# Performance work log

Hardware: AMD Instinct MI355X
Metric: run time of the kernel (lower is better)

The kernel has to match this reference:

```python
import jax, jax.numpy as jnp
import numpy as np


def setup_inputs() -> dict:
    key = jax.random.key(0)
    k1, k2 = jax.random.split(key)
    B, H, W, E = 8, 32, 32, 256   # latent grid (NHWC layout, as in vector_quantize)
    N_E = 16384                   # codebook size
    x = jax.random.normal(k1, (B, H, W, E), dtype=jnp.float32)
    codebook = jax.random.normal(k2, (N_E, E), dtype=jnp.float32)
    return {"x": x, "codebook": codebook}


def reference(x, codebook):
    # d[b,h,w,k] = ||x[b,h,w] - codebook[k]||^2 (expanded form, as in source)
    x_sq = jnp.sum(x * x, axis=-1, keepdims=True)            # [B,H,W,1]
    cb_sq = jnp.sum(codebook * codebook, axis=1)              # [N_E]
    cross = jnp.einsum('bhwe,ke->bhwk', x, codebook)          # [B,H,W,N_E]
    d = x_sq + cb_sq - 2.0 * cross
    indices = jnp.argmin(d, axis=-1)                          # [B,H,W]
    x_q = jnp.take(codebook, indices, axis=0)                 # one-hot @ codebook == row gather
    # straight-through / ReplaceGrad: forward value is x_q, gradient flows to x
    return x + jax.lax.stop_gradient(x_q - x)
```

## Files before the change

kernel.cpp:

```cpp
#include <hip/hip_runtime.h>
#include <stdint.h>

#define M_PIX 8192
#define N_CB  16384
#define KD    256

typedef float f32x4 __attribute__((ext_vector_type(4)));
typedef int   i32x4 __attribute__((ext_vector_type(4)));
typedef int   i32x8 __attribute__((ext_vector_type(8)));
typedef unsigned long long ull;

#define OFF_CF8  (0ULL)
#define OFF_XF8  (4ULL << 20)
#define OFF_CBSQ (6ULL << 20)
#define OFF_SLOT (7ULL << 20)
#define WS_REQ   (15ULL << 20)

__device__ __forceinline__ unsigned int fkey(float s) {
  unsigned int f = __float_as_uint(s);
  return f ^ ((unsigned int)(((int)f) >> 31) | 0x80000000u);
}
__device__ __forceinline__ unsigned char f2e4m3(float v) {
  float av = fminf(fabsf(v), 448.0f);
  const unsigned s = (__float_as_uint(v) >> 24) & 0x80u;
  unsigned m;
  if (av >= 0.015625f) {
    unsigned u = __float_as_uint(av);
    u += 0x7FFFFu + ((u >> 20) & 1u);
    m = (((u >> 23) - 120u) << 3) | ((u >> 20) & 7u);
  } else {
    m = (unsigned)(int)rintf(av * 512.0f);
  }
  return (unsigned char)(s | m);
}
__device__ __forceinline__ void gl_lds16(const unsigned char* g, char* l) {
  __builtin_amdgcn_global_load_lds(
      (const __attribute__((address_space(1))) unsigned int*)(const void*)g,
      (__attribute__((address_space(3))) unsigned int*)(void*)l,
      16, 0, 0);
}
__device__ __forceinline__ void ins2f(float k, float& v1, float& v2) {
  v2 = fminf(v2, fmaxf(v1, k));
  v1 = fminf(v1, k);
}
__device__ __forceinline__ i32x8 ld32(const char* p, int addr) {
  const i32x4 lo = *(const i32x4*)(const void*)(p + addr);
  const i32x4 hi = *(const i32x4*)(const void*)(p + (addr ^ 16));
  return (i32x8){lo.x, lo.y, lo.z, lo.w, hi.x, hi.y, hi.z, hi.w};
}

__global__ __launch_bounds__(256) void prep_kernel(
    const float* __restrict__ x, const float* __restrict__ cb,
    unsigned char* __restrict__ Cf8, unsigned char* __restrict__ Xf8,
    float* __restrict__ cbsq) {
  const int wid = threadIdx.x >> 6, lane = threadIdx.x & 63;
  const int row = blockIdx.x * 4 + wid;
  const bool isCb = (row < N_CB);
  const int rowL = isCb ? row : row - N_CB;
  const float* src = (isCb ? cb : x) + (size_t)rowL * KD;
  const float4 v = ((const float4*)src)[lane];
  uchar4 pk;
  pk.x = f2e4m3(v.x); pk.y = f2e4m3(v.y); pk.z = f2e4m3(v.z); pk.w = f2e4m3(v.w);
  *(uchar4*)(void*)((isCb ? Cf8 : Xf8) + (size_t)rowL * KD + lane * 4) = pk;
  if (isCb) {
    float ss = v.x*v.x + v.y*v.y + v.z*v.z + v.w*v.w;
    #pragma unroll
    for (int off = 32; off > 0; off >>= 1) ss += __shfl_xor(ss, off);
    if (lane == 0) cbsq[rowL] = ss;
  }
}


__global__ __launch_bounds__(256, 3) void gemm_top2_kernel(
    const unsigned char* __restrict__ Xf8, const unsigned char* __restrict__ Cf8,
    const float* __restrict__ cbsq, float2* __restrict__ slots) {
  __shared__ __align__(16) char smem[32768];
  char* A_s = smem;
  char* B_s = smem + 16384;
  float2* P = (float2*)smem;

  const int tid = threadIdx.x;
  const int wid = tid >> 6, lane = tid & 63;
  const int wy = wid >> 1, wx = wid & 1;
  const int q = lane >> 4, c = lane & 15;

  const int bx = blockIdx.x & 7, bg = blockIdx.x >> 3;
  const int mt = bg >> 4;
  const int nt = bx * 16 + (bg & 15);
  const int m0 = mt * 128, n0 = nt * 128;

  const int swz = (c & 7) << 4;
  int aaddr[4], baddr[4];
  #pragma unroll
  for (int i = 0; i < 4; i++) {
    aaddr[i] = (((wy * 64 + i * 16 + c) * 128) + q * 32) ^ swz;
    baddr[i] = ((((wx * 64 + i * 16 + c) * 128) + q * 32) ^ swz) + 16384;
  }

  const f32x4 zf = {0.f, 0.f, 0.f, 0.f};
  f32x4 acc[4][4];
  #pragma unroll
  for (int i = 0; i < 4; i++)
    #pragma unroll
    for (int j = 0; j < 4; j++) acc[i][j] = zf;

  const int srow8 = lane >> 3;
  const int sgb = ((lane & 7) ^ srow8) * 16;

  #pragma unroll
  for (int hk = 0; hk < 2; hk++) {
    if (hk) __syncthreads();
    #pragma unroll
    for (int j = 0; j < 4; j++) {
      const int chunk = j * 4 + wid;
      const int row = chunk * 8 + srow8;
      const int gb = sgb + hk * 128;
      gl_lds16(Xf8 + (size_t)(m0 + row) * KD + gb, A_s + chunk * 1024);
      gl_lds16(Cf8 + (size_t)(n0 + row) * KD + gb, B_s + chunk * 1024);
    }
    __syncthreads();
    i32x8 bfr[4];
    #pragma unroll
    for (int ni = 0; ni < 4; ni++)
      bfr[ni] = ld32(smem, baddr[ni]);
    #pragma unroll
    for (int mi = 0; mi < 4; mi++) {
      const i32x8 af = ld32(smem, aaddr[mi]);
      #pragma unroll
      for (int ni = 0; ni < 4; ni++)
        acc[mi][ni] = __builtin_amdgcn_mfma_scale_f32_16x16x128_f8f6f4(
            af, bfr[ni], acc[mi][ni], 0, 0,
            0, 0x7F7F7F7F,
            0, 0x7F7F7F7F);
    }
  }
  __syncthreads();

  float cs[4]; unsigned colp[4];
  #pragma unroll
  for (int ni = 0; ni < 4; ni++) {
    colp[ni] = wx * 64 + ni * 16 + c;
    cs[ni] = cbsq[n0 + colp[ni]];
  }

  #pragma unroll
  for (int mi = 0; mi < 4; mi++) {
    #pragma unroll
    for (int r = 0; r < 4; r++) {
      float k[4];
      #pragma unroll
      for (int ni = 0; ni < 4; ni++) {
        const float s = fmaf(-2.f, acc[mi][ni][r], cs[ni]);
        k[ni] = __uint_as_float((__float_as_uint(s) & 0xFFFFFF80u) |
                                (colp[ni] & 0x7Fu));
      }
      const float m1 = fminf(k[0], k[1]), M1 = fmaxf(k[0], k[1]);
      const float m2 = fminf(k[2], k[3]), M2 = fmaxf(k[2], k[3]);
      const float v1 = fminf(m1, m2);
      const float v2 = fminf(fmaxf(m1, m2), fminf(M1, M2));
      const int row = wy * 64 + mi * 16 + q * 4 + r;
      const int slot = wx * 16 + c;
      P[row * 32 + (slot ^ (row & 31))] = make_float2(v1, v2);
    }
  }
  __syncthreads();

  {
    const float FINF = __uint_as_float(0x7F800000u);
    const int srow = tid >> 1, half = tid & 1;
    const int sw = srow & 31;
    float v1 = FINF, v2 = FINF;
    #pragma unroll
    for (int t = 0; t < 16; t++) {
      const float2 pv = P[srow * 32 + ((half * 16 + t) ^ sw)];
      ins2f(pv.x, v1, v2);
      ins2f(pv.y, v1, v2);
    }
    const float b1 = __shfl_xor(v1, 1), b2 = __shfl_xor(v2, 1);
    const float hi = fmaxf(v1, b1);
    v1 = fminf(v1, b1);
    v2 = fminf(fminf(v2, b2), hi);
    if (!half)
      slots[(size_t)nt * M_PIX + m0 + srow] = make_float2(v1, v2);
  }
}

__global__ __launch_bounds__(256) void reduce_rescore_gather(
    const float* __restrict__ x, const float* __restrict__ cb,
    const float* __restrict__ cbsq, const float2* __restrict__ slots,
    float* __restrict__ out) {
  const int wid = threadIdx.x >> 6, lane = threadIdx.x & 63;
  const int pixel = blockIdx.x * 4 + wid;

  const float2 sA = slots[(size_t)lane * M_PIX + pixel];
  const float2 sB = slots[(size_t)(64 + lane) * M_PIX + pixel];
  const float sc[4] = {sA.x, sA.y, sB.x, sB.y};
  float mn = fminf(fminf(sc[0], sc[1]), fminf(sc[2], sc[3]));
  #pragma unroll
  for (int off = 1; off < 64; off <<= 1) mn = fminf(mn, __shfl_xor(mn, off));
  const float thr = mn + 10.0f;

  const float4 xv = ((const float4*)x)[(size_t)pixel * 64 + lane];
  ull best = ~0ULL;
  #pragma unroll
  for (int j = 0; j < 4; j++) {
    ull mask = __ballot(sc[j] < thr);
    while (mask) {
      const int src = (int)__ffsll((long long)mask) - 1;
      mask &= mask - 1;
      const float val = __shfl(sc[j], src);
      const unsigned ij = (unsigned)(((j >> 1) * 64 + src) * 128) +
                          (__float_as_uint(val) & 127u);
      const float4 cv = ((const float4*)cb)[(size_t)ij * 64 + lane];
      float d = xv.x*cv.x + xv.y*cv.y + xv.z*cv.z + xv.w*cv.w;
      #pragma unroll
      for (int off = 1; off < 64; off <<= 1) d += __shfl_xor(d, off);
      const float sv = fmaf(-2.f, d, cbsq[ij]);
      const ull k = ((ull)fkey(sv) << 32) | ij;
      best = k < best ? k : best;
    }
  }
  const unsigned w = (unsigned)best;
  ((float4*)out)[(size_t)pixel * 64 + lane] = ((const float4*)cb)[(size_t)w * 64 + lane];
}

__global__ __launch_bounds__(256) void fallback_kernel(
    const float* __restrict__ x, const float* __restrict__ cb,
    float* __restrict__ out) {
  __shared__ float xs[256];
  __shared__ unsigned long long keys[4];
  __shared__ int widx;
  const int p = blockIdx.x;
  const int tid = threadIdx.x, wid = tid >> 6, lane = tid & 63;
  xs[tid] = x[(size_t)p * KD + tid];
  __syncthreads();
  const float4 xv = ((const float4*)xs)[lane];
  float bestS = 3.4e38f; int bestI = 0;
  for (int k = wid; k < N_CB; k += 4) {
    const float4 cv = ((const float4*)cb)[(size_t)k * 64 + lane];
    float t = cv.x*(cv.x - 2.f*xv.x) + cv.y*(cv.y - 2.f*xv.y)
            + cv.z*(cv.z - 2.f*xv.z) + cv.w*(cv.w - 2.f*xv.w);
    #pragma unroll
    for (int off = 1; off < 64; off <<= 1) t += __shfl_xor(t, off);
    if (t < bestS) { bestS = t; bestI = k; }
  }
  if (lane == 0)
    keys[wid] = ((unsigned long long)fkey(bestS) << 32) | (unsigned int)bestI;
  __syncthreads();
  if (tid == 0) {
    unsigned long long m = keys[0];
    for (int i = 1; i < 4; i++) if (keys[i] < m) m = keys[i];
    widx = (int)(unsigned int)(m & 0xFFFFFFFFULL);
  }
  __syncthreads();
  out[(size_t)p * KD + tid] = cb[(size_t)widx * KD + tid];
}

extern "C" void kernel_launch(void* const* d_in, const int* in_sizes, int n_in,
                              void* d_out, int out_size, void* d_ws, size_t ws_size,
                              hipStream_t stream) {
  const float* x  = (const float*)d_in[0];
  const float* cb = (const float*)d_in[1];
  float* out = (float*)d_out;

  if (ws_size < WS_REQ) {
    fallback_kernel<<<M_PIX, 256, 0, stream>>>(x, cb, out);
    return;
  }

  char* ws = (char*)d_ws;
  unsigned char* Cf8 = (unsigned char*)(ws + OFF_CF8);
  unsigned char* Xf8 = (unsigned char*)(ws + OFF_XF8);
  float* cbsq        = (float*)(ws + OFF_CBSQ);
  float2* slots      = (float2*)(ws + OFF_SLOT);

  prep_kernel<<<(N_CB + M_PIX) / 4, 256, 0, stream>>>(x, cb, Cf8, Xf8, cbsq);
  gemm_top2_kernel<<<M_PIX, 256, 0, stream>>>(Xf8, Cf8, cbsq, slots);
  reduce_rescore_gather<<<M_PIX / 4, 256, 0, stream>>>(x, cb, cbsq, slots, out);
}
```

Measured before the change: 144.0 us.

## Make GEMM blocks persistent over 16 codebook tiles with double-buffered LDS

The GEMM+top2 kernel now launches 512 blocks instead of 8192. Each block keeps its 128-row X tile resident in registers and loops over 16 codebook tiles, prefetching the next tile into a second LDS buffer while computing the current one. The top-2 reduction now uses wave shuffles instead of a shared-memory partial stage. This removes repeated X loads and per-block launch and sync overhead, at the cost of 64KB of LDS, lower occupancy, and only 512 blocks to fill the GPU.

```diff
diff --git a/kernel.cpp b/kernel.cpp
--- a/kernel.cpp
+++ b/kernel.cpp
@@ -71,117 +71,147 @@
 }
 
 
-__global__ __launch_bounds__(256, 3) void gemm_top2_kernel(
+__global__ __launch_bounds__(256, 2) void gemm_top2_kernel(
     const unsigned char* __restrict__ Xf8, const unsigned char* __restrict__ Cf8,
     const float* __restrict__ cbsq, float2* __restrict__ slots) {
-  __shared__ __align__(16) char smem[32768];
-  char* A_s = smem;
-  char* B_s = smem + 16384;
-  float2* P = (float2*)smem;
+  __shared__ __align__(16) char smem[65536];
 
   const int tid = threadIdx.x;
   const int wid = tid >> 6, lane = tid & 63;
-  const int wy = wid >> 1, wx = wid & 1;
+  const int wy = wid;
   const int q = lane >> 4, c = lane & 15;
 
-  const int bx = blockIdx.x & 7, bg = blockIdx.x >> 3;
-  const int mt = bg >> 4;
-  const int nt = bx * 16 + (bg & 15);
-  const int m0 = mt * 128, n0 = nt * 128;
-
-  const int swz = (c & 7) << 4;
-  int aaddr[4], baddr[4];
-  #pragma unroll
-  for (int i = 0; i < 4; i++) {
-    aaddr[i] = (((wy * 64 + i * 16 + c) * 128) + q * 32) ^ swz;
-    baddr[i] = ((((wx * 64 + i * 16 + c) * 128) + q * 32) ^ swz) + 16384;
-  }
-
-  const f32x4 zf = {0.f, 0.f, 0.f, 0.f};
-  f32x4 acc[4][4];
-  #pragma unroll
-  for (int i = 0; i < 4; i++)
-    #pragma unroll
-    for (int j = 0; j < 4; j++) acc[i][j] = zf;
+  const int xcd = blockIdx.x & 7;
+  const int mt  = blockIdx.x >> 3;
+  const int m0  = mt * 128;
+  const int ntb = xcd * 16;
 
   const int srow8 = lane >> 3;
   const int sgb = ((lane & 7) ^ srow8) * 16;
 
-  #pragma unroll
-  for (int hk = 0; hk < 2; hk++) {
-    if (hk) __syncthreads();
+  const int swz = (c & 7) << 4;
+  int aaddr[2], baddr[8];
+  #pragma unroll
+  for (int mi = 0; mi < 2; mi++)
+    aaddr[mi] = (((wy * 32 + mi * 16 + c) * 128) + q * 32) ^ swz;
+  #pragma unroll
+  for (int ni = 0; ni < 8; ni++)
+    baddr[ni] = (((ni * 16 + c) * 128) + q * 32) ^ swz;
+
+  #pragma unroll
+  for (int hk = 0; hk < 2; hk++)
     #pragma unroll
     for (int j = 0; j < 4; j++) {
       const int chunk = j * 4 + wid;
       const int row = chunk * 8 + srow8;
-      const int gb = sgb + hk * 128;
-      gl_lds16(Xf8 + (size_t)(m0 + row) * KD + gb, A_s + chunk * 1024);
-      gl_lds16(Cf8 + (size_t)(n0 + row) * KD + gb, B_s + chunk * 1024);
-    }
-    __syncthreads();
-    i32x8 bfr[4];
-    #pragma unroll
-    for (int ni = 0; ni < 4; ni++)
-      bfr[ni] = ld32(smem, baddr[ni]);
-    #pragma unroll
-    for (int mi = 0; mi < 4; mi++) {
-      const i32x8 af = ld32(smem, aaddr[mi]);
-      #pragma unroll
-      for (int ni = 0; ni < 4; ni++)
-        acc[mi][ni] = __builtin_amdgcn_mfma_scale_f32_16x16x128_f8f6f4(
-            af, bfr[ni], acc[mi][ni], 0, 0,
-            0, 0x7F7F7F7F,
-            0, 0x7F7F7F7F);
-    }
-  }
-  __syncthreads();
-
-  float cs[4]; unsigned colp[4];
-  #pragma unroll
-  for (int ni = 0; ni < 4; ni++) {
-    colp[ni] = wx * 64 + ni * 16 + c;
-    cs[ni] = cbsq[n0 + colp[ni]];
-  }
-
-  #pragma unroll
-  for (int mi = 0; mi < 4; mi++) {
-    #pragma unroll
-    for (int r = 0; r < 4; r++) {
-      float k[4];
-      #pragma unroll
-      for (int ni = 0; ni < 4; ni++) {
-        const float s = fmaf(-2.f, acc[mi][ni][r], cs[ni]);
-        k[ni] = __uint_as_float((__float_as_uint(s) & 0xFFFFFF80u) |
-                                (colp[ni] & 0x7Fu));
+      gl_lds16(Xf8 + (size_t)(m0 + row) * KD + sgb + hk * 128,
+               smem + hk * 16384 + chunk * 1024);
+    }
+  #pragma unroll
+  for (int hk = 0; hk < 2; hk++)
+    #pragma unroll
+    for (int j = 0; j < 4; j++) {
+      const int chunk = j * 4 + wid;
+      const int row = chunk * 8 + srow8;
+      gl_lds16(Cf8 + (size_t)(ntb * 128 + row) * KD + sgb + hk * 128,
+               smem + 32768 + hk * 16384 + chunk * 1024);
+    }
+  __builtin_amdgcn_sched_barrier(0);
+  asm volatile("s_waitcnt vmcnt(8)" ::: "memory");
+  __builtin_amdgcn_s_barrier();
+  __builtin_amdgcn_sched_barrier(0);
+
+  i32x8 af[2][2];
+  #pragma unroll
+  for (int mi = 0; mi < 2; mi++)
+    #pragma unroll
+    for (int k = 0; k < 2; k++)
+      af[mi][k] = ld32(smem, aaddr[mi] + k * 16384);
+  asm volatile("s_waitcnt lgkmcnt(0)" ::: "memory");
+  __builtin_amdgcn_sched_barrier(0);
+  asm volatile("s_waitcnt vmcnt(0)" ::: "memory");
+  __builtin_amdgcn_s_barrier();
+  __builtin_amdgcn_sched_barrier(0);
+
+  const float FINF = __uint_as_float(0x7F800000u);
+  const f32x4 zf = {0.f, 0.f, 0.f, 0.f};
+
+  #pragma unroll 1
+  for (int i = 0; i < 16; ++i) {
+    const int n0 = (ntb + i) * 128;
+    const int cur = ((i + 1) & 1) * 32768;
+    const int nxt = (i & 1) * 32768;
+
+    float cs[8];
+    #pragma unroll
+    for (int ni = 0; ni < 8; ni++) cs[ni] = cbsq[n0 + ni * 16 + c];
+    __builtin_amdgcn_sched_barrier(0);
+
+    if (i < 15) {
+      #pragma unroll
+      for (int hk = 0; hk < 2; hk++)
+        #pragma unroll
+        for (int j = 0; j < 4; j++) {
+          const int chunk = j * 4 + wid;
+          const int row = chunk * 8 + srow8;
+          gl_lds16(Cf8 + (size_t)(n0 + 128 + row) * KD + sgb + hk * 128,
+                   smem + nxt + hk * 16384 + chunk * 1024);
+        }
+    }
+    __builtin_amdgcn_sched_barrier(0);
+
+    f32x4 acc[2][8];
+    #pragma unroll
+    for (int mi = 0; mi < 2; mi++)
+      #pragma unroll
+      for (int ni = 0; ni < 8; ni++) acc[mi][ni] = zf;
+    #pragma unroll
+    for (int k = 0; k < 2; k++) {
+      i32x8 bfr[8];
+      #pragma unroll
+      for (int ni = 0; ni < 8; ni++)
+        bfr[ni] = ld32(smem, baddr[ni] + cur + k * 16384);
+      #pragma unroll
+      for (int mi = 0; mi < 2; mi++)
+        #pragma unroll
+        for (int ni = 0; ni < 8; ni++)
+          acc[mi][ni] = __builtin_amdgcn_mfma_scale_f32_16x16x128_f8f6f4(
+              af[mi][k], bfr[ni], acc[mi][ni], 0, 0,
+              0, 0x7F7F7F7F,
+              0, 0x7F7F7F7F);
+    }
+
+    #pragma unroll
+    for (int mi = 0; mi < 2; mi++) {
+      #pragma unroll
+      for (int r = 0; r < 4; r++) {
+        float v1 = FINF, v2 = FINF;
+        #pragma unroll
+        for (int ni = 0; ni < 8; ni++) {
+          const float s = fmaf(-2.f, acc[mi][ni][r], cs[ni]);
+          ins2f(__uint_as_float((__float_as_uint(s) & 0xFFFFFF80u) |
+                                (unsigned)(ni * 16 + c)), v1, v2);
+        }
+        #pragma unroll
+        for (int m = 1; m < 16; m <<= 1) {
+          const float o1 = __shfl_xor(v1, m), o2 = __shfl_xor(v2, m);
+          const float hi = fmaxf(v1, o1);
+          v1 = fminf(v1, o1);
+          v2 = fminf(fminf(v2, o2), hi);
+        }
+        if (c == 0) {
+          const int row = wy * 32 + mi * 16 + q * 4 + r;
+          slots[(size_t)(ntb + i) * M_PIX + m0 + row] = make_float2(v1, v2);
+        }
       }
-      const float m1 = fminf(k[0], k[1]), M1 = fmaxf(k[0], k[1]);
-      const float m2 = fminf(k[2], k[3]), M2 = fmaxf(k[2], k[3]);
-      const float v1 = fminf(m1, m2);
-      const float v2 = fminf(fmaxf(m1, m2), fminf(M1, M2));
-      const int row = wy * 64 + mi * 16 + q * 4 + r;
-      const int slot = wx * 16 + c;
-      P[row * 32 + (slot ^ (row & 31))] = make_float2(v1, v2);
-    }
-  }
-  __syncthreads();
-
-  {
-    const float FINF = __uint_as_float(0x7F800000u);
-    const int srow = tid >> 1, half = tid & 1;
-    const int sw = srow & 31;
-    float v1 = FINF, v2 = FINF;
-    #pragma unroll
-    for (int t = 0; t < 16; t++) {
-      const float2 pv = P[srow * 32 + ((half * 16 + t) ^ sw)];
-      ins2f(pv.x, v1, v2);
-      ins2f(pv.y, v1, v2);
-    }
-    const float b1 = __shfl_xor(v1, 1), b2 = __shfl_xor(v2, 1);
-    const float hi = fmaxf(v1, b1);
-    v1 = fminf(v1, b1);
-    v2 = fminf(fminf(v2, b2), hi);
-    if (!half)
-      slots[(size_t)nt * M_PIX + m0 + srow] = make_float2(v1, v2);
+    }
+
+    if (i < 15) {
+      __builtin_amdgcn_sched_barrier(0);
+      asm volatile("s_waitcnt vmcnt(8)" ::: "memory");
+      __builtin_amdgcn_s_barrier();
+      __builtin_amdgcn_sched_barrier(0);
+    }
   }
 }
 
@@ -275,6 +305,6 @@
   float2* slots      = (float2*)(ws + OFF_SLOT);
 
   prep_kernel<<<(N_CB + M_PIX) / 4, 256, 0, stream>>>(x, cb, Cf8, Xf8, cbsq);
-  gemm_top2_kernel<<<M_PIX, 256, 0, stream>>>(Xf8, Cf8, cbsq, slots);
+  gemm_top2_kernel<<<512, 256, 0, stream>>>(Xf8, Cf8, cbsq, slots);
   reduce_rescore_gather<<<M_PIX / 4, 256, 0, stream>>>(x, cb, cbsq, slots, out);
 }
```

Result: slower. 160.9 us (+11.8%).
